# Performance work log

Hardware: AMD Instinct MI355X
Metric: run time of the kernel (lower is better)

The kernel has to match this reference:

```python
import jax, jax.numpy as jnp
import numpy as np
import math

B, NQ, NK, D = 8, 2048, 2048, 512
EPS = 1e-8


def setup_inputs() -> dict:
    key = jax.random.key(0)
    k1, k2, k3 = jax.random.split(key, 3)
    qs = jax.random.normal(k1, (B, NQ, D), dtype=jnp.float32)
    ks = jax.random.normal(k2, (B, NK, D), dtype=jnp.float32)
    vs = jax.random.normal(k3, (B, NK, D), dtype=jnp.float32)
    scale = jnp.full((1,), math.sqrt(D), dtype=jnp.float32)  # nn.Parameter(sqrt(dim))
    bias = jnp.zeros((), dtype=jnp.float32)
    return {"qs": qs, "ks": ks, "vs": vs, "scale": scale, "bias": bias}


def _lorentz_self_inner(u):
    # <u,u>_L = -u0^2 + sum_{i>0} u_i^2 = sum u_i^2 - 2*u0^2, keepdim on last axis
    return jnp.sum(u * u, axis=-1, keepdims=True) - 2.0 * (u[..., :1] ** 2)


def reference(qs, ks, vs, scale, bias):
    # cinner: Minkowski inner product, time coord (index 0) sign-flipped on qs
    q_flip = qs.at[..., 0].multiply(-1.0)
    att = -jnp.einsum('bqd,bkd->bqk', q_flip, ks)  # -cinner(qs, ks)
    att = jax.nn.softmax(att / scale + bias, axis=-1)
    # Einstein/Lorentz midpoint: weighted sum then renormalize to the hyperboloid (k=1)
    ave = jnp.einsum('bqk,bkd->bqd', att, vs)
    denom = jnp.sqrt(jnp.clip(jnp.abs(-_lorentz_self_inner(ave)), EPS, None))
    return ave / denom
```

## Files before the change

### kernel.cpp

```cpp
#include <hip/hip_runtime.h>

#define NSEQ 2048
#define DIM  512
#define KVBLK 32
#define NKT  64
#define TILEB 32768
#define SMEMB (4 * TILEB + 4096)

typedef __bf16 bf16x8 __attribute__((ext_vector_type(8)));
typedef float  f32x4  __attribute__((ext_vector_type(4)));

__device__ __forceinline__ void gld16(const void* g, void* l) {
  __builtin_amdgcn_global_load_lds(
      (const __attribute__((address_space(1))) unsigned int*)g,
      (__attribute__((address_space(3))) unsigned int*)l, 16, 0, 0);
}

__global__ __launch_bounds__(256) void prep_k(const float* __restrict__ ks,
                                              char* __restrict__ kp) {
  int b = blockIdx.x >> 6, kt = blockIdx.x & 63;
  int t = threadIdx.x;
  const float* src = ks + ((size_t)(b * NSEQ + kt * KVBLK)) * DIM;
  char* dst = kp + ((size_t)(b * 64 + kt)) * TILEB;
#pragma unroll
  for (int i = 0; i < 8; ++i) {
    int c = t + i * 256;
    int row = c >> 6;
    int d0 = (c & 63) * 8;
    const float4* s4 = (const float4*)(src + row * DIM + d0);
    float4 x = s4[0], y = s4[1];
    bf16x8 h;
    h[0] = (__bf16)x.x; h[1] = (__bf16)x.y; h[2] = (__bf16)x.z; h[3] = (__bf16)x.w;
    h[4] = (__bf16)y.x; h[5] = (__bf16)y.y; h[6] = (__bf16)y.z; h[7] = (__bf16)y.w;
    *(bf16x8*)(dst + row * 1024 + ((d0 * 2) ^ ((row & 7) << 4))) = h;
  }
}

__global__ __launch_bounds__(256) void prep_v(const float* __restrict__ vs,
                                              char* __restrict__ vtp) {
  __shared__ __align__(16) char lds[TILEB];
  int b = blockIdx.x >> 6, kt = blockIdx.x & 63;
  int t = threadIdx.x;
  const float* src = vs + ((size_t)(b * NSEQ + kt * KVBLK)) * DIM;
#pragma unroll
  for (int i = 0; i < 8; ++i) {
    int c = t + i * 256;
    int kv = c >> 6;
    int d0 = (c & 63) * 8;
    const float4* s4 = (const float4*)(src + kv * DIM + d0);
    float4 x = s4[0], y = s4[1];
    float vals[8] = {x.x, x.y, x.z, x.w, y.x, y.y, y.z, y.w};
#pragma unroll
    for (int j = 0; j < 8; ++j) {
      int d = d0 + j;
      int byte = (d >> 1) * 128 + (((((d & 1) * 64) + kv * 2)) ^ (((d >> 1) & 7) << 4));
      *(__bf16*)(lds + byte) = (__bf16)vals[j];
    }
  }
  __syncthreads();
  char* dst = vtp + ((size_t)(b * 64 + kt)) * TILEB;
#pragma unroll
  for (int i = 0; i < 8; ++i) {
    int c16 = t + i * 256;
    *(bf16x8*)(dst + c16 * 16) = *(const bf16x8*)(lds + c16 * 16);
  }
}

__global__ __launch_bounds__(256) void attn_main(
    const float* __restrict__ qs, const char* __restrict__ kp,
    const char* __restrict__ vtp, const float* __restrict__ scale,
    float* __restrict__ out) {
  extern __shared__ __align__(16) char smem[];
  int b  = blockIdx.x & 7;
  int qt = blockIdx.x >> 3;
  int tid = threadIdx.x;
  int w = tid >> 6, lane = tid & 63;
  int c = lane & 15, g = lane >> 4;
  int q0 = qt * 64 + w * 16;

  char* kb0 = smem;
  char* kb1 = smem + TILEB;
  char* vb0 = smem + 2 * TILEB;
  char* vb1 = smem + 3 * TILEB;
  char* plds = smem + 4 * TILEB + w * 1024;

  float cc = 1.4426950408889634f / scale[0];

  bf16x8 qf[16];
#pragma unroll
  for (int k = 0; k < 16; ++k) {
    int d = k * 32 + g * 8;
    const float4* p = (const float4*)(qs + ((size_t)(b * NSEQ + q0 + c)) * DIM + d);
    float4 x = p[0], y = p[1];
    float vals[8] = {x.x, x.y, x.z, x.w, y.x, y.y, y.z, y.w};
    bf16x8 h;
#pragma unroll
    for (int j = 0; j < 8; ++j) {
      float mlt = (d + j == 0) ? cc : -cc;
      h[j] = (__bf16)(vals[j] * mlt);
    }
    qf[k] = h;
  }

  f32x4 acc[32];
#pragma unroll
  for (int i = 0; i < 32; ++i) acc[i] = (f32x4){0.f, 0.f, 0.f, 0.f};
  float mrow = -1e30f;

  const char* kpb = kp  + (size_t)b * 64 * TILEB;
  const char* vpb = vtp + (size_t)b * 64 * TILEB;

#pragma unroll
  for (int i = 0; i < 8; ++i) {
    int o = tid * 16 + i * 4096;
    gld16(kpb + o, kb0 + o);
    gld16(vpb + o, vb0 + o);
  }
  __syncthreads();

  const int csw = (c & 7) << 4;
  const int vt_lane = (c >> 1) * 128 +
      (((((c & 1) * 64) + g * 16)) ^ (((c >> 1) & 7) << 4));
  const int qb = (c >> 1) * 128;
  const int qh = (c & 1) * 64;
  const int qx = ((c >> 1) & 7) << 4;

  for (int t = 0; t < NKT; ++t) {
    char* kb = (t & 1) ? kb1 : kb0;
    char* vb = (t & 1) ? vb1 : vb0;
    if (t + 1 < NKT) {
      char* kn = (t & 1) ? kb0 : kb1;
      char* vn = (t & 1) ? vb0 : vb1;
      const char* ksrc = kpb + (size_t)(t + 1) * TILEB;
      const char* vsrc = vpb + (size_t)(t + 1) * TILEB;
#pragma unroll
      for (int i = 0; i < 8; ++i) {
        int o = tid * 16 + i * 4096;
        gld16(ksrc + o, kn + o);
        gld16(vsrc + o, vn + o);
      }
    }

    f32x4 sa0 = {0.f,0.f,0.f,0.f}, sb0 = {0.f,0.f,0.f,0.f};
    f32x4 sa1 = {0.f,0.f,0.f,0.f}, sb1 = {0.f,0.f,0.f,0.f};
    const char* krl = kb + c * 1024;
    const char* krh = krl + 16 * 1024;
#pragma unroll
    for (int k = 0; k < 16; ++k) {
      int bir = (k * 64 + g * 16) ^ csw;
      bf16x8 kfl = *(const bf16x8*)(krl + bir);
      bf16x8 kfh = *(const bf16x8*)(krh + bir);
      if (k & 1) {
        sb0 = __builtin_amdgcn_mfma_f32_16x16x32_bf16(kfl, qf[k], sb0, 0, 0, 0);
        sb1 = __builtin_amdgcn_mfma_f32_16x16x32_bf16(kfh, qf[k], sb1, 0, 0, 0);
      } else {
        sa0 = __builtin_amdgcn_mfma_f32_16x16x32_bf16(kfl, qf[k], sa0, 0, 0, 0);
        sa1 = __builtin_amdgcn_mfma_f32_16x16x32_bf16(kfh, qf[k], sa1, 0, 0, 0);
      }
    }
    f32x4 sl = sa0 + sb0;
    f32x4 sh = sa1 + sb1;

    float mm = fmaxf(fmaxf(fmaxf(sl[0], sl[1]), fmaxf(sl[2], sl[3])),
                     fmaxf(fmaxf(sh[0], sh[1]), fmaxf(sh[2], sh[3])));
    mm = fmaxf(mm, __shfl_xor(mm, 16));
    mm = fmaxf(mm, __shfl_xor(mm, 32));
    if (__any(mm > mrow + 11.0f)) {
      float mn = fmaxf(mrow, mm);
      float f = exp2f(mrow - mn);
      mrow = mn;
      float f0 = __shfl(f, 4 * g + 0), f1 = __shfl(f, 4 * g + 1);
      float f2 = __shfl(f, 4 * g + 2), f3 = __shfl(f, 4 * g + 3);
#pragma unroll
      for (int i = 0; i < 32; ++i) {
        acc[i][0] *= f0; acc[i][1] *= f1; acc[i][2] *= f2; acc[i][3] *= f3;
      }
    }

#pragma unroll
    for (int r = 0; r < 4; ++r) {
      float pvl = exp2f(sl[r] - mrow);
      float pvh = exp2f(sh[r] - mrow);
      int kvl = 4 * g + r;
      *(__bf16*)(plds + qb + ((qh + kvl * 2) ^ qx))        = (__bf16)pvl;
      *(__bf16*)(plds + qb + ((qh + (16 + kvl) * 2) ^ qx)) = (__bf16)pvh;
    }
    bf16x8 pf = *(const bf16x8*)(plds + vt_lane);

    const char* vr = vb + vt_lane;
#pragma unroll
    for (int dtl = 0; dtl < 32; ++dtl) {
      bf16x8 vf = *(const bf16x8*)(vr + dtl * 1024);
      acc[dtl] = __builtin_amdgcn_mfma_f32_16x16x32_bf16(pf, vf, acc[dtl], 0, 0, 0);
    }
    __syncthreads();
  }

#pragma unroll
  for (int r = 0; r < 4; ++r) {
    float ss = 0.f;
#pragma unroll
    for (int dtl = 0; dtl < 32; ++dtl) ss += acc[dtl][r] * acc[dtl][r];
    ss += __shfl_xor(ss, 1);
    ss += __shfl_xor(ss, 2);
    ss += __shfl_xor(ss, 4);
    ss += __shfl_xor(ss, 8);
    float a0 = __shfl(acc[0][r], lane & 48);
    float d2 = fabsf(2.f * a0 * a0 - ss);
    float inv = rsqrtf(fmaxf(d2, 1e-8f));
    float* orow = out + ((size_t)(b * NSEQ + q0 + 4 * g + r)) * DIM + c;
#pragma unroll
    for (int dtl = 0; dtl < 32; ++dtl) orow[dtl * 16] = acc[dtl][r] * inv;
  }
}

extern "C" void kernel_launch(void* const* d_in, const int* in_sizes, int n_in,
                              void* d_out, int out_size, void* d_ws, size_t ws_size,
                              hipStream_t stream) {
  (void)in_sizes; (void)n_in; (void)out_size;
  const float* qs = (const float*)d_in[0];
  const float* ks = (const float*)d_in[1];
  const float* vs = (const float*)d_in[2];
  const float* scale = (const float*)d_in[3];
  float* out = (float*)d_out;

  size_t need = (size_t)2 * 8 * 64 * TILEB;
  if (ws_size < need) return;
  char* kp  = (char*)d_ws;
  char* vtp = (char*)d_ws + (size_t)8 * 64 * TILEB;

  hipFuncSetAttribute((const void*)attn_main,
                      hipFuncAttributeMaxDynamicSharedMemorySize, SMEMB);

  prep_k<<<512, 256, 0, stream>>>(ks, kp);
  prep_v<<<512, 256, 0, stream>>>(vs, vtp);
  attn_main<<<256, 256, SMEMB, stream>>>(qs, kp, vtp, scale, out);
}
```

Baseline: 167.3 us.

## Software-pipeline QK of next tile with PV of current tile

The main loop is restructured so that each iteration computes the QK scores for tile t+1 while it accumulates P·V for tile t, interleaving the two sets of MFMAs. A prologue handles the QK and softmax of the first tile, and an epilogue handles the last P·V. The K and V prefetches are decoupled so that K runs two tiles ahead and V one tile ahead, using the same double-buffered LDS. The goal is to hide the softmax and exp latency and the serial dependency between the two matmuls, at the cost of more live registers and a more complex buffer schedule.

```diff
diff --git a/kernel.cpp b/kernel.cpp
--- a/kernel.cpp
+++ b/kernel.cpp
@@ -78,10 +78,8 @@
   int c = lane & 15, g = lane >> 4;
   int q0 = qt * 64 + w * 16;
 
-  char* kb0 = smem;
-  char* kb1 = smem + TILEB;
-  char* vb0 = smem + 2 * TILEB;
-  char* vb1 = smem + 3 * TILEB;
+  char* kbuf = smem;
+  char* vbuf = smem + 2 * TILEB;
   char* plds = smem + 4 * TILEB + w * 1024;
 
   float cc = 1.4426950408889634f / scale[0];
@@ -110,14 +108,6 @@
   const char* kpb = kp  + (size_t)b * 64 * TILEB;
   const char* vpb = vtp + (size_t)b * 64 * TILEB;
 
-#pragma unroll
-  for (int i = 0; i < 8; ++i) {
-    int o = tid * 16 + i * 4096;
-    gld16(kpb + o, kb0 + o);
-    gld16(vpb + o, vb0 + o);
-  }
-  __syncthreads();
-
   const int csw = (c & 7) << 4;
   const int vt_lane = (c >> 1) * 128 +
       (((((c & 1) * 64) + g * 16)) ^ (((c >> 1) & 7) << 4));
@@ -125,25 +115,22 @@
   const int qh = (c & 1) * 64;
   const int qx = ((c >> 1) & 7) << 4;
 
-  for (int t = 0; t < NKT; ++t) {
-    char* kb = (t & 1) ? kb1 : kb0;
-    char* vb = (t & 1) ? vb1 : vb0;
-    if (t + 1 < NKT) {
-      char* kn = (t & 1) ? kb0 : kb1;
-      char* vn = (t & 1) ? vb0 : vb1;
-      const char* ksrc = kpb + (size_t)(t + 1) * TILEB;
-      const char* vsrc = vpb + (size_t)(t + 1) * TILEB;
-#pragma unroll
-      for (int i = 0; i < 8; ++i) {
-        int o = tid * 16 + i * 4096;
-        gld16(ksrc + o, kn + o);
-        gld16(vsrc + o, vn + o);
-      }
-    }
-
+#pragma unroll
+  for (int i = 0; i < 8; ++i) {
+    int o = tid * 16 + i * 4096;
+    gld16(kpb + o, kbuf + o);
+    gld16(vpb + o, vbuf + o);
+    gld16(kpb + TILEB + o, kbuf + TILEB + o);
+  }
+  __syncthreads();
+
+  f32x4 sl, sh;
+  bf16x8 pf;
+
+  {
     f32x4 sa0 = {0.f,0.f,0.f,0.f}, sb0 = {0.f,0.f,0.f,0.f};
     f32x4 sa1 = {0.f,0.f,0.f,0.f}, sb1 = {0.f,0.f,0.f,0.f};
-    const char* krl = kb + c * 1024;
+    const char* krl = kbuf + c * 1024;
     const char* krh = krl + 16 * 1024;
 #pragma unroll
     for (int k = 0; k < 16; ++k) {
@@ -158,8 +145,67 @@
         sa1 = __builtin_amdgcn_mfma_f32_16x16x32_bf16(kfh, qf[k], sa1, 0, 0, 0);
       }
     }
-    f32x4 sl = sa0 + sb0;
-    f32x4 sh = sa1 + sb1;
+    sl = sa0 + sb0; sh = sa1 + sb1;
+    float mm = fmaxf(fmaxf(fmaxf(sl[0], sl[1]), fmaxf(sl[2], sl[3])),
+                     fmaxf(fmaxf(sh[0], sh[1]), fmaxf(sh[2], sh[3])));
+    mm = fmaxf(mm, __shfl_xor(mm, 16));
+    mm = fmaxf(mm, __shfl_xor(mm, 32));
+    mrow = mm;
+#pragma unroll
+    for (int r = 0; r < 4; ++r) {
+      float pvl = exp2f(sl[r] - mrow);
+      float pvh = exp2f(sh[r] - mrow);
+      int kvl = 4 * g + r;
+      *(__bf16*)(plds + qb + ((qh + kvl * 2) ^ qx))        = (__bf16)pvl;
+      *(__bf16*)(plds + qb + ((qh + (16 + kvl) * 2) ^ qx)) = (__bf16)pvh;
+    }
+    pf = *(const bf16x8*)(plds + vt_lane);
+  }
+  __syncthreads();
+
+  for (int t = 0; t < NKT - 1; ++t) {
+    if (t + 2 < NKT) {
+      const char* ksrc = kpb + (size_t)(t + 2) * TILEB;
+      char* kdst = kbuf + (t & 1) * TILEB;
+#pragma unroll
+      for (int i = 0; i < 8; ++i) {
+        int o = tid * 16 + i * 4096;
+        gld16(ksrc + o, kdst + o);
+      }
+    }
+    {
+      const char* vsrc = vpb + (size_t)(t + 1) * TILEB;
+      char* vdst = vbuf + ((t + 1) & 1) * TILEB;
+#pragma unroll
+      for (int i = 0; i < 8; ++i) {
+        int o = tid * 16 + i * 4096;
+        gld16(vsrc + o, vdst + o);
+      }
+    }
+
+    f32x4 sa0 = {0.f,0.f,0.f,0.f}, sb0 = {0.f,0.f,0.f,0.f};
+    f32x4 sa1 = {0.f,0.f,0.f,0.f}, sb1 = {0.f,0.f,0.f,0.f};
+    const char* krl = kbuf + ((t + 1) & 1) * TILEB + c * 1024;
+    const char* krh = krl + 16 * 1024;
+    const char* vr  = vbuf + (t & 1) * TILEB + vt_lane;
+#pragma unroll
+    for (int k = 0; k < 16; ++k) {
+      int bir = (k * 64 + g * 16) ^ csw;
+      bf16x8 kfl = *(const bf16x8*)(krl + bir);
+      bf16x8 kfh = *(const bf16x8*)(krh + bir);
+      bf16x8 vf0 = *(const bf16x8*)(vr + (2 * k) * 1024);
+      bf16x8 vf1 = *(const bf16x8*)(vr + (2 * k + 1) * 1024);
+      if (k & 1) {
+        sb0 = __builtin_amdgcn_mfma_f32_16x16x32_bf16(kfl, qf[k], sb0, 0, 0, 0);
+        sb1 = __builtin_amdgcn_mfma_f32_16x16x32_bf16(kfh, qf[k], sb1, 0, 0, 0);
+      } else {
+        sa0 = __builtin_amdgcn_mfma_f32_16x16x32_bf16(kfl, qf[k], sa0, 0, 0, 0);
+        sa1 = __builtin_amdgcn_mfma_f32_16x16x32_bf16(kfh, qf[k], sa1, 0, 0, 0);
+      }
+      acc[2 * k]     = __builtin_amdgcn_mfma_f32_16x16x32_bf16(pf, vf0, acc[2 * k], 0, 0, 0);
+      acc[2 * k + 1] = __builtin_amdgcn_mfma_f32_16x16x32_bf16(pf, vf1, acc[2 * k + 1], 0, 0, 0);
+    }
+    sl = sa0 + sb0; sh = sa1 + sb1;
 
     float mm = fmaxf(fmaxf(fmaxf(sl[0], sl[1]), fmaxf(sl[2], sl[3])),
                      fmaxf(fmaxf(sh[0], sh[1]), fmaxf(sh[2], sh[3])));
@@ -185,15 +231,18 @@
       *(__bf16*)(plds + qb + ((qh + kvl * 2) ^ qx))        = (__bf16)pvl;
       *(__bf16*)(plds + qb + ((qh + (16 + kvl) * 2) ^ qx)) = (__bf16)pvh;
     }
-    bf16x8 pf = *(const bf16x8*)(plds + vt_lane);
-
-    const char* vr = vb + vt_lane;
+    pf = *(const bf16x8*)(plds + vt_lane);
+
+    __syncthreads();
+  }
+
+  {
+    const char* vr = vbuf + ((NKT - 1) & 1) * TILEB + vt_lane;
 #pragma unroll
     for (int dtl = 0; dtl < 32; ++dtl) {
       bf16x8 vf = *(const bf16x8*)(vr + dtl * 1024);
       acc[dtl] = __builtin_amdgcn_mfma_f32_16x16x32_bf16(pf, vf, acc[dtl], 0, 0, 0);
     }
-    __syncthreads();
   }
 
 #pragma unroll
```

Measured after the change: 154.9 us. 7.4% less time.
